# Optimization experiments

Hardware: AMD Instinct MI355X
Metric: run time of the kernel (lower is better)

The kernel has to match this reference:

```python
import jax, jax.numpy as jnp
import numpy as np

B = 8          # batch instances
EPS = 1e-6     # stable instance norm epsilon


def sparse_conv(x, nbr, W):
    """Kernel-map sparse conv: out[n] = sum_k x[nbr[n,k]] @ W[k].
    x: [N,Cin], nbr: [N,K] int, W: [K,Cin,Cout]. Scan over the K=27 kernel
    offsets keeps the gathered intermediate at [N,Cin] per step."""
    init = jnp.zeros((x.shape[0], W.shape[-1]), x.dtype)

    def body(acc, wk_nk):
        w, nk = wk_nk
        return acc + x[nk] @ w, None

    acc, _ = jax.lax.scan(body, init, (W, nbr.T))
    return acc


def instance_norm(x, batch_idx):
    """MinkowskiStableInstanceNorm: per-instance, per-channel (x-mean)/sqrt(var+eps)."""
    ones = jnp.ones((x.shape[0], 1), x.dtype)
    cnt = jnp.maximum(jax.ops.segment_sum(ones, batch_idx, num_segments=B), 1.0)  # [B,1]
    mean = jax.ops.segment_sum(x, batch_idx, num_segments=B) / cnt               # [B,C]
    xc = x - mean[batch_idx]
    var = jax.ops.segment_sum(xc * xc, batch_idx, num_segments=B) / cnt          # [B,C]
    return xc * jax.lax.rsqrt(var + EPS)[batch_idx]


def setup_inputs() -> dict:
    key = jax.random.key(0)
    ks = jax.random.split(key, 8)
    N, C, K, E = 131072, 128, 27, 512
    x = jax.random.normal(ks[0], (N, C), jnp.float32)
    emb = jax.random.normal(ks[1], (B, E), jnp.float32)
    batch_idx = jnp.sort(jax.random.randint(ks[2], (N,), 0, B)).astype(jnp.int32)
    nbr = jax.random.randint(ks[3], (N, K), 0, N).astype(jnp.int32)
    s = 1.0 / np.sqrt(C * K)
    W1 = jax.random.normal(ks[4], (K, C, C), jnp.float32) * s
    W2 = jax.random.normal(ks[5], (K, C, C), jnp.float32) * s
    Wt = jax.random.normal(ks[6], (E, 2 * C), jnp.float32) * (1.0 / np.sqrt(E))
    bt = jnp.zeros((2 * C,), jnp.float32)
    return {"x_feats": x, "emb": emb, "W1": W1, "W2": W2, "Wt": Wt, "bt": bt,
            "batch_idx": batch_idx, "nbr": nbr}


def reference(x_feats, emb, W1, W2, Wt, bt, batch_idx, nbr):
    # conv1 -> stable instance norm -> scale_shift time-emb injection
    out = sparse_conv(x_feats, nbr, W1)
    out = instance_norm(out, batch_idx)
    C = out.shape[1]
    e = (emb @ Wt + bt)[batch_idx]          # gather per-point time emb [N, 2C]
    scale, shift = e[:, :C], e[:, C:]
    out = out * (1.0 + scale) + shift
    out = jax.nn.elu(out)
    # conv2 -> norm2 -> residual -> ELU
    out = sparse_conv(out, nbr, W2)
    out = instance_norm(out, batch_idx)
    out = out + x_feats
    return jax.nn.elu(out)
```

## Files before the change

### kernel.cpp

```cpp
#include <hip/hip_runtime.h>
#include <hip/hip_bf16.h>

typedef __bf16 bf16x8 __attribute__((ext_vector_type(8)));
typedef float  f32x4  __attribute__((ext_vector_type(4)));

#define GAS __attribute__((address_space(1)))
#define LAS __attribute__((address_space(3)))

__device__ __forceinline__ unsigned short f2bf(float f) {
    __hip_bfloat16 h = __float2bfloat16(f);
    return *reinterpret_cast<unsigned short*>(&h);
}
__device__ __forceinline__ float bf2f(unsigned short u) {
    __hip_bfloat16 h;
    *reinterpret_cast<unsigned short*>(&h) = u;
    return __bfloat162float(h);
}
__device__ __forceinline__ void storeval(float* p, float v) { *p = v; }
__device__ __forceinline__ void storeval(unsigned short* p, float v) { *p = f2bf(v); }

__global__ void prep_x_kernel(const float* __restrict__ in, unsigned short* __restrict__ out, int total) {
    int idx = (blockIdx.x * 256 + threadIdx.x) * 4;
    if (idx >= total) return;
    float4 v = *reinterpret_cast<const float4*>(in + idx);
    ushort4 o;
    o.x = f2bf(v.x); o.y = f2bf(v.y); o.z = f2bf(v.z); o.w = f2bf(v.w);
    *reinterpret_cast<ushort4*>(out + idx) = o;
}

__global__ void prep_w_kernel(const float* __restrict__ W, unsigned short* __restrict__ Wp) {
    int idx = blockIdx.x * 256 + threadIdx.x;
    int k  = idx >> 14;
    int r  = idx & 16383;
    int h  = r >> 13;
    int rr = r & 8191;
    int co = rr >> 6;
    int cc = rr & 63;
    int c8 = cc >> 3, j = cc & 7;
    int ci = (h << 6) | ((c8 ^ (co & 7)) << 3) | j;
    Wp[idx] = f2bf(W[(k << 14) + ci * 128 + co]);
}

__global__ void film_kernel(const float* __restrict__ emb, const float* __restrict__ Wt,
                            const float* __restrict__ bt, float* __restrict__ e) {
    int gw = blockIdx.x * 4 + (threadIdx.x >> 6);
    int lane = threadIdx.x & 63;
    int b = gw >> 8, j = gw & 255;
    float a = 0.f;
    for (int i = lane; i < 512; i += 64) a += emb[b * 512 + i] * Wt[i * 256 + j];
#pragma unroll
    for (int off = 32; off; off >>= 1) a += __shfl_xor(a, off);
    if (lane == 0) e[gw] = a + bt[j];
}

template <typename OUT_T>
__global__ __launch_bounds__(256, 2) void conv_kernel(
        const unsigned short* __restrict__ X,
        const int* __restrict__ nbr,
        const unsigned short* __restrict__ Wp,
        OUT_T* __restrict__ out,
        const int* __restrict__ bidx,
        float* __restrict__ gsum, float* __restrict__ gsq, float* __restrict__ gcnt,
        int N) {
    __shared__ __align__(16) unsigned short As[2][128 * 64];
    __shared__ __align__(16) unsigned short Bs[2][128 * 64];
    __shared__ int nbrS[128 * 27];
    __shared__ float ssum[2][128];
    __shared__ float ssq[2][128];
    __shared__ float shi;

    const int t = threadIdx.x;
    const int lane = t & 63;
    const int wave = t >> 6;
    const int n0 = blockIdx.x * 128;

    for (int i = t; i < 128 * 27; i += 256) nbrS[i] = nbr[(size_t)n0 * 27 + i];
    if (t < 128) { ssum[0][t] = 0.f; ssum[1][t] = 0.f; ssq[0][t] = 0.f; ssq[1][t] = 0.f; }
    if (t == 0) shi = 0.f;

    f32x4 acc[4][4];
#pragma unroll
    for (int mi = 0; mi < 4; mi++)
#pragma unroll
        for (int ni = 0; ni < 4; ni++) acc[mi][ni] = (f32x4){0.f, 0.f, 0.f, 0.f};

    const int wr = wave >> 1, wc = wave & 1;
    const int l15 = lane & 15, l4 = lane >> 4;

    auto stage = [&](int sidx) {
        const int h1 = sidx >= 27 ? 1 : 0;
        const int k1 = sidx - h1 * 27;
        unsigned short* Ad = &As[sidx & 1][0];
        unsigned short* Bd = &Bs[sidx & 1][0];
#pragma unroll
        for (int i = 0; i < 4; ++i) {
            int chunk = i * 256 + t;
            int row = chunk >> 3;
            int c8 = chunk & 7;
            int g = c8 ^ (row & 7);
            int srow = nbrS[row * 27 + k1];
            __builtin_amdgcn_global_load_lds(
                (const GAS void*)(X + (size_t)srow * 128 + h1 * 64 + g * 8),
                (LAS void*)(Ad + (size_t)(i * 256 + wave * 64) * 8), 16, 0, 0);
        }
        const unsigned short* wsrc = Wp + (size_t)(k1 * 2 + h1) * 8192;
#pragma unroll
        for (int i = 0; i < 4; ++i) {
            __builtin_amdgcn_global_load_lds(
                (const GAS void*)(wsrc + (size_t)(i * 256 + t) * 8),
                (LAS void*)(Bd + (size_t)(i * 256 + wave * 64) * 8), 16, 0, 0);
        }
    };
    auto computeStep = [&](int buf) {
#pragma unroll
        for (int kk = 0; kk < 2; ++kk) {
            const int c8 = kk * 4 + l4;
            bf16x8 a[4], b[4];
#pragma unroll
            for (int mi = 0; mi < 4; mi++) {
                int row = wr * 64 + mi * 16 + l15;
                a[mi] = *reinterpret_cast<const bf16x8*>(&As[buf][row * 64 + (c8 ^ (row & 7)) * 8]);
            }
#pragma unroll
            for (int ni = 0; ni < 4; ni++) {
                int co = wc * 64 + ni * 16 + l15;
                b[ni] = *reinterpret_cast<const bf16x8*>(&Bs[buf][co * 64 + (c8 ^ (co & 7)) * 8]);
            }
#pragma unroll
            for (int mi = 0; mi < 4; mi++)
#pragma unroll
                for (int ni = 0; ni < 4; ni++)
                    acc[mi][ni] = __builtin_amdgcn_mfma_f32_16x16x32_bf16(a[mi], b[ni], acc[mi][ni], 0, 0, 0);
        }
    };

    __syncthreads();
    stage(0);

    for (int s = 0; s < 53; ++s) {
        stage(s + 1);
        __builtin_amdgcn_sched_barrier(0);
        asm volatile("s_waitcnt vmcnt(8)" ::: "memory");
        __builtin_amdgcn_sched_barrier(0);
        __builtin_amdgcn_s_barrier();
        __builtin_amdgcn_sched_barrier(0);
        computeStep(s & 1);
        __builtin_amdgcn_sched_barrier(0);
        __builtin_amdgcn_s_barrier();
        __builtin_amdgcn_sched_barrier(0);
    }
    asm volatile("s_waitcnt vmcnt(0)" ::: "memory");
    __builtin_amdgcn_sched_barrier(0);
    __builtin_amdgcn_s_barrier();
    __builtin_amdgcn_sched_barrier(0);
    computeStep(1);

    const int b_lo = bidx[n0];
    const int b_hi = bidx[n0 + 127];
    const bool split = (b_hi != b_lo);

    float ps0[4] = {0.f, 0.f, 0.f, 0.f}, ps1[4] = {0.f, 0.f, 0.f, 0.f};
    float pq0[4] = {0.f, 0.f, 0.f, 0.f}, pq1[4] = {0.f, 0.f, 0.f, 0.f};
#pragma unroll
    for (int mi = 0; mi < 4; mi++) {
#pragma unroll
        for (int j = 0; j < 4; j++) {
            int rowm = wr * 64 + mi * 16 + l4 * 4 + j;
            bool hi = split && (bidx[n0 + rowm] != b_lo);
#pragma unroll
            for (int ni = 0; ni < 4; ni++) {
                float v = acc[mi][ni][j];
                float v1 = hi ? v : 0.f;
                float v0 = v - v1;
                ps0[ni] += v0; pq0[ni] += v0 * v;
                ps1[ni] += v1; pq1[ni] += v1 * v;
                int col = wc * 64 + ni * 16 + l15;
                storeval(out + (size_t)(n0 + rowm) * 128 + col, v);
            }
        }
    }
#pragma unroll
    for (int ni = 0; ni < 4; ni++) {
        int col = wc * 64 + ni * 16 + l15;
        atomicAdd(&ssum[0][col], ps0[ni]);
        atomicAdd(&ssq[0][col], pq0[ni]);
        if (split) {
            atomicAdd(&ssum[1][col], ps1[ni]);
            atomicAdd(&ssq[1][col], pq1[ni]);
        }
    }
    if (split && wave < 2) {
        bool hi = (bidx[n0 + t] != b_lo);
        unsigned long long m = __ballot(hi);
        if (lane == 0) atomicAdd(&shi, (float)__popcll(m));
    }
    __syncthreads();
    {
        int slot = t >> 7, c = t & 127;
        if (slot == 0 || split) {
            int b = slot ? b_hi : b_lo;
            atomicAdd(&gsum[b * 128 + c], ssum[slot][c]);
            atomicAdd(&gsq[b * 128 + c], ssq[slot][c]);
        }
        if (t == 0) {
            float nhi = shi;
            atomicAdd(&gcnt[b_lo], 128.f - nhi);
            if (split) atomicAdd(&gcnt[b_hi], nhi);
        }
    }
}

__global__ void apply1_kernel(const unsigned short* __restrict__ o1, const int* __restrict__ bidx,
                              const float* __restrict__ gsum, const float* __restrict__ gsq,
                              const float* __restrict__ gcnt, const float* __restrict__ e,
                              unsigned short* __restrict__ y, int N) {
    int idx = blockIdx.x * 256 + threadIdx.x;
    int n = idx >> 5;
    if (n >= N) return;
    int c0 = (idx & 31) << 2;
    int b = bidx[n];
    float icnt = 1.0f / fmaxf(gcnt[b], 1.0f);
    ushort4 vv = *reinterpret_cast<const ushort4*>(o1 + (size_t)n * 128 + c0);
    const unsigned short* pv = reinterpret_cast<const unsigned short*>(&vv);
    unsigned short res[4];
#pragma unroll
    for (int j = 0; j < 4; j++) {
        int c = c0 + j;
        float m = gsum[b * 128 + c] * icnt;
        float var = gsq[b * 128 + c] * icnt - m * m;
        float rs = rsqrtf(fmaxf(var, 0.f) + 1e-6f);
        float xn = (bf2f(pv[j]) - m) * rs;
        float sc = e[b * 256 + c];
        float sh = e[b * 256 + 128 + c];
        float tt = xn * (1.0f + sc) + sh;
        float r = tt > 0.f ? tt : expm1f(tt);
        res[j] = f2bf(r);
    }
    *reinterpret_cast<ushort4*>(y + (size_t)n * 128 + c0) = *reinterpret_cast<ushort4*>(res);
}

__global__ void apply2_kernel(float* __restrict__ o2, const float* __restrict__ xf,
                              const int* __restrict__ bidx, const float* __restrict__ gsum,
                              const float* __restrict__ gsq, const float* __restrict__ gcnt, int N) {
    int idx = blockIdx.x * 256 + threadIdx.x;
    int n = idx >> 5;
    if (n >= N) return;
    int c0 = (idx & 31) << 2;
    int b = bidx[n];
    float icnt = 1.0f / fmaxf(gcnt[b], 1.0f);
    float4 v = *reinterpret_cast<const float4*>(o2 + (size_t)n * 128 + c0);
    float4 xv = *reinterpret_cast<const float4*>(xf + (size_t)n * 128 + c0);
    const float* pv = reinterpret_cast<const float*>(&v);
    const float* px = reinterpret_cast<const float*>(&xv);
    float res[4];
#pragma unroll
    for (int j = 0; j < 4; j++) {
        int c = c0 + j;
        float m = gsum[b * 128 + c] * icnt;
        float var = gsq[b * 128 + c] * icnt - m * m;
        float rs = rsqrtf(fmaxf(var, 0.f) + 1e-6f);
        float zn = (pv[j] - m) * rs;
        float r2 = zn + px[j];
        res[j] = r2 > 0.f ? r2 : expm1f(r2);
    }
    *reinterpret_cast<float4*>(o2 + (size_t)n * 128 + c0) =
        *reinterpret_cast<float4*>(res);
}

extern "C" void kernel_launch(void* const* d_in, const int* in_sizes, int n_in,
                              void* d_out, int out_size, void* d_ws, size_t ws_size,
                              hipStream_t stream) {
    const float* x    = (const float*)d_in[0];
    const float* emb  = (const float*)d_in[1];
    const float* W1   = (const float*)d_in[2];
    const float* W2   = (const float*)d_in[3];
    const float* Wt   = (const float*)d_in[4];
    const float* bt   = (const float*)d_in[5];
    const int* bidx   = (const int*)d_in[6];
    const int* nbr    = (const int*)d_in[7];
    float* out        = (float*)d_out;
    const int N = in_sizes[0] / 128;

    char* ws = (char*)d_ws;
    unsigned short* xb  = (unsigned short*)ws;
    unsigned short* o1b = (unsigned short*)(ws + (size_t)N * 256);
    unsigned short* w1p = (unsigned short*)(ws + (size_t)N * 512);
    unsigned short* w2p = w1p + 27 * 16384;
    float* e    = (float*)(w2p + 27 * 16384);
    float* st   = e + 2048;
    float* sum1 = st;
    float* sq1  = st + 1024;
    float* cnt1 = st + 2048;
    float* sum2 = st + 2056;
    float* sq2  = st + 3080;
    float* cnt2 = st + 4104;

    hipMemsetAsync(st, 0, 4112 * sizeof(float), stream);

    int total = N * 128;
    prep_x_kernel<<<(total / 4 + 255) / 256, 256, 0, stream>>>(x, xb, total);
    prep_w_kernel<<<27 * 64, 256, 0, stream>>>(W1, w1p);
    prep_w_kernel<<<27 * 64, 256, 0, stream>>>(W2, w2p);
    film_kernel<<<512, 256, 0, stream>>>(emb, Wt, bt, e);

    conv_kernel<unsigned short><<<N / 128, 256, 0, stream>>>(xb, nbr, w1p, o1b, bidx, sum1, sq1, cnt1, N);
    apply1_kernel<<<(N * 32 + 255) / 256, 256, 0, stream>>>(o1b, bidx, sum1, sq1, cnt1, e, xb, N);

    conv_kernel<float><<<N / 128, 256, 0, stream>>>(xb, nbr, w2p, out, bidx, sum2, sq2, cnt2, N);
    apply2_kernel<<<(N * 32 + 255) / 256, 256, 0, stream>>>(out, x, bidx, sum2, sq2, cnt2, N);
}
```

Measured before the change: 438.4 us.

## Deepen conv gather pipeline to four stages with 32-channel K slices

```diff
diff --git a/kernel.cpp b/kernel.cpp
--- a/kernel.cpp
+++ b/kernel.cpp
@@ -30,14 +30,12 @@
 
 __global__ void prep_w_kernel(const float* __restrict__ W, unsigned short* __restrict__ Wp) {
     int idx = blockIdx.x * 256 + threadIdx.x;
-    int k  = idx >> 14;
-    int r  = idx & 16383;
-    int h  = r >> 13;
-    int rr = r & 8191;
-    int co = rr >> 6;
-    int cc = rr & 63;
-    int c8 = cc >> 3, j = cc & 7;
-    int ci = (h << 6) | ((c8 ^ (co & 7)) << 3) | j;
+    int cc = idx & 31;
+    int co = (idx >> 5) & 127;
+    int kq = idx >> 12;
+    int k  = kq >> 2, q = kq & 3;
+    int c4 = cc >> 3, j = cc & 7;
+    int ci = (q << 5) | ((c4 ^ (co & 3)) << 3) | j;
     Wp[idx] = f2bf(W[(k << 14) + ci * 128 + co]);
 }
 
@@ -62,8 +60,8 @@
         const int* __restrict__ bidx,
         float* __restrict__ gsum, float* __restrict__ gsq, float* __restrict__ gcnt,
         int N) {
-    __shared__ __align__(16) unsigned short As[2][128 * 64];
-    __shared__ __align__(16) unsigned short Bs[2][128 * 64];
+    __shared__ __align__(16) unsigned short As[4][128 * 32];
+    __shared__ __align__(16) unsigned short Bs[4][128 * 32];
     __shared__ int nbrS[128 * 27];
     __shared__ float ssum[2][128];
     __shared__ float ssq[2][128];
@@ -87,73 +85,88 @@
     const int wr = wave >> 1, wc = wave & 1;
     const int l15 = lane & 15, l4 = lane >> 4;
 
-    auto stage = [&](int sidx) {
-        const int h1 = sidx >= 27 ? 1 : 0;
-        const int k1 = sidx - h1 * 27;
-        unsigned short* Ad = &As[sidx & 1][0];
-        unsigned short* Bd = &Bs[sidx & 1][0];
-#pragma unroll
-        for (int i = 0; i < 4; ++i) {
-            int chunk = i * 256 + t;
-            int row = chunk >> 3;
-            int c8 = chunk & 7;
-            int g = c8 ^ (row & 7);
+    auto stage = [&](int sidx, int slot) {
+        const int k1 = sidx >> 2, q1 = sidx & 3;
+        unsigned short* Ad = &As[slot][0];
+        unsigned short* Bd = &Bs[slot][0];
+#pragma unroll
+        for (int i = 0; i < 2; ++i) {
+            int c = i * 256 + t;
+            int row = c >> 2;
+            int c4 = c & 3;
+            int g = c4 ^ (row & 3);
             int srow = nbrS[row * 27 + k1];
             __builtin_amdgcn_global_load_lds(
-                (const GAS void*)(X + (size_t)srow * 128 + h1 * 64 + g * 8),
+                (const GAS void*)(X + (size_t)srow * 128 + q1 * 32 + g * 8),
                 (LAS void*)(Ad + (size_t)(i * 256 + wave * 64) * 8), 16, 0, 0);
         }
-        const unsigned short* wsrc = Wp + (size_t)(k1 * 2 + h1) * 8192;
-#pragma unroll
-        for (int i = 0; i < 4; ++i) {
+        const unsigned short* wsrc = Wp + (size_t)sidx * 4096;
+#pragma unroll
+        for (int i = 0; i < 2; ++i) {
             __builtin_amdgcn_global_load_lds(
                 (const GAS void*)(wsrc + (size_t)(i * 256 + t) * 8),
                 (LAS void*)(Bd + (size_t)(i * 256 + wave * 64) * 8), 16, 0, 0);
         }
     };
-    auto computeStep = [&](int buf) {
-#pragma unroll
-        for (int kk = 0; kk < 2; ++kk) {
-            const int c8 = kk * 4 + l4;
-            bf16x8 a[4], b[4];
-#pragma unroll
-            for (int mi = 0; mi < 4; mi++) {
-                int row = wr * 64 + mi * 16 + l15;
-                a[mi] = *reinterpret_cast<const bf16x8*>(&As[buf][row * 64 + (c8 ^ (row & 7)) * 8]);
-            }
-#pragma unroll
-            for (int ni = 0; ni < 4; ni++) {
-                int co = wc * 64 + ni * 16 + l15;
-                b[ni] = *reinterpret_cast<const bf16x8*>(&Bs[buf][co * 64 + (c8 ^ (co & 7)) * 8]);
-            }
-#pragma unroll
-            for (int mi = 0; mi < 4; mi++)
-#pragma unroll
-                for (int ni = 0; ni < 4; ni++)
-                    acc[mi][ni] = __builtin_amdgcn_mfma_f32_16x16x32_bf16(a[mi], b[ni], acc[mi][ni], 0, 0, 0);
-        }
+    auto computeStep = [&](int slot) {
+        bf16x8 a[4], b[4];
+#pragma unroll
+        for (int mi = 0; mi < 4; mi++) {
+            int row = wr * 64 + mi * 16 + l15;
+            a[mi] = *reinterpret_cast<const bf16x8*>(&As[slot][row * 32 + ((l4 ^ (row & 3)) * 8)]);
+        }
+#pragma unroll
+        for (int ni = 0; ni < 4; ni++) {
+            int co = wc * 64 + ni * 16 + l15;
+            b[ni] = *reinterpret_cast<const bf16x8*>(&Bs[slot][co * 32 + ((l4 ^ (co & 3)) * 8)]);
+        }
+#pragma unroll
+        for (int mi = 0; mi < 4; mi++)
+#pragma unroll
+            for (int ni = 0; ni < 4; ni++)
+                acc[mi][ni] = __builtin_amdgcn_mfma_f32_16x16x32_bf16(a[mi], b[ni], acc[mi][ni], 0, 0, 0);
     };
 
     __syncthreads();
-    stage(0);
-
-    for (int s = 0; s < 53; ++s) {
-        stage(s + 1);
-        __builtin_amdgcn_sched_barrier(0);
-        asm volatile("s_waitcnt vmcnt(8)" ::: "memory");
-        __builtin_amdgcn_sched_barrier(0);
-        __builtin_amdgcn_s_barrier();
-        __builtin_amdgcn_sched_barrier(0);
-        computeStep(s & 1);
-        __builtin_amdgcn_sched_barrier(0);
-        __builtin_amdgcn_s_barrier();
-        __builtin_amdgcn_sched_barrier(0);
-    }
+    stage(0, 0);
+    stage(1, 1);
+    stage(2, 2);
+
+#define STEP(S, CSLOT, SSLOT)                                                  \
+    {                                                                          \
+        stage((S) + 3, SSLOT);                               \
+        __builtin_amdgcn_sched_barrier(0);                                     \
+        asm volatile("s_waitcnt vmcnt(12)" ::: "memory");  \
+        __builtin_amdgcn_sched_barrier(0);                                     \
+        __builtin_amdgcn_s_barrier();       \
+        __builtin_amdgcn_sched_barrier(0);                                     \
+        computeStep(CSLOT);                                                    \
+        __builtin_amdgcn_sched_barrier(0);                                     \
+        __builtin_amdgcn_s_barrier();                 \
+        __builtin_amdgcn_sched_barrier(0);                                     \
+    }
+
+    for (int s = 0; s < 104; s += 4) {
+        STEP(s + 0, 0, 3);
+        STEP(s + 1, 1, 0);
+        STEP(s + 2, 2, 1);
+        STEP(s + 3, 3, 2);
+    }
+    STEP(104, 0, 3);
+#undef STEP
+
+    asm volatile("s_waitcnt vmcnt(8)" ::: "memory");
+    __builtin_amdgcn_sched_barrier(0);
+    __builtin_amdgcn_s_barrier();
+    computeStep(1);
+    asm volatile("s_waitcnt vmcnt(4)" ::: "memory");
+    __builtin_amdgcn_sched_barrier(0);
+    __builtin_amdgcn_s_barrier();
+    computeStep(2);
     asm volatile("s_waitcnt vmcnt(0)" ::: "memory");
     __builtin_amdgcn_sched_barrier(0);
     __builtin_amdgcn_s_barrier();
-    __builtin_amdgcn_sched_barrier(0);
-    computeStep(1);
+    computeStep(3);
 
     const int b_lo = bidx[n0];
     const int b_hi = bidx[n0 + 127];
```

Result: slower. 513.3 us (+17.1%).
